# Kernel optimization log

Hardware: AMD Instinct MI355X
Metric: run time of the kernel (lower is better)

Reference implementation:

```python
import jax, jax.numpy as jnp
import numpy as np

B, C_IN, C_OUT, K, IN_SIZE = 16, 32, 32, 16, 8192
OUT_SIZE = IN_SIZE - K  # 8176


def setup_inputs() -> dict:
    key = jax.random.key(0)
    kx, kw, kb = jax.random.split(key, 3)
    x = jax.random.normal(kx, (B, C_IN, IN_SIZE), dtype=jnp.float32)
    # locally-connected (non-weight-shared) conv weights generated by cppn at init
    w = jax.random.normal(kw, (C_OUT, C_IN, OUT_SIZE, K), dtype=jnp.float32)
    b = jax.random.normal(kb, (C_OUT,), dtype=jnp.float32)
    return {"x": x, "w": w, "b": b}


def reference(x, w, b):
    # sliding-window gather: idxs[o, t] = o + t, shape (O, K)
    idxs = jnp.arange(OUT_SIZE)[:, None] + jnp.arange(K)[None, :]
    windows = x[:, :, idxs]  # (B, C_in, O, K)
    # per-output-position weights: contract over C_in and K only
    out = jnp.einsum("bcok,dcok->bdo", windows, w)  # (B, C_out, O)
    return jax.nn.relu(out + b[None, :, None])
```

## Files before the change

### kernel.cpp

```cpp
#include <hip/hip_runtime.h>
#include <cstddef>

constexpr int Bn  = 16;
constexpr int CIc = 32;
constexpr int COc = 32;
constexpr int Kc  = 16;
constexpr int IN  = 8192;
constexpr int OUTL = 8176;

constexpr int O_B  = 16;
constexpr int CCH  = 8;
constexpr int NPOS = O_B + Kc - 1;
constexpr int BST  = 20;

__global__ __launch_bounds__(256, 2)
void conv1d_cppn_kernel(const float* __restrict__ x, const float* __restrict__ w,
                        const float* __restrict__ bias, float* __restrict__ out) {
    __shared__ float xs[CCH][NPOS][BST];

    const int tid = threadIdx.x;
    const int og = tid & 15;
    const int dg = tid >> 4;
    const int o0 = blockIdx.x * O_B;
    const int o  = o0 + og;
    const int dbase = dg * 2;

    float acc[2][16];
#pragma unroll
    for (int i = 0; i < 2; ++i)
#pragma unroll
        for (int j = 0; j < 16; ++j) acc[i][j] = 0.f;

    for (int chunk = 0; chunk < CIc / CCH; ++chunk) {
        const int c0 = chunk * CCH;
        __syncthreads();
        for (int idx = tid; idx < CCH * Bn * NPOS; idx += 256) {
            const int p  = idx % NPOS;
            const int t  = idx / NPOS;
            const int b  = t & 15;
            const int cc = t >> 4;
            xs[cc][p][b] = x[((size_t)b * CIc + (c0 + cc)) * IN + o0 + p];
        }
        __syncthreads();

#pragma unroll 2
        for (int cc = 0; cc < CCH; ++cc) {
            const int c = c0 + cc;
            float wreg[2][16];
#pragma unroll
            for (int jd = 0; jd < 2; ++jd) {
                const float4* wp = reinterpret_cast<const float4*>(
                    w + (((size_t)(dbase + jd) * CIc + c) * OUTL + o) * Kc);
#pragma unroll
                for (int q = 0; q < 4; ++q) {
                    const float4 v = wp[q];
                    wreg[jd][q * 4 + 0] = v.x;
                    wreg[jd][q * 4 + 1] = v.y;
                    wreg[jd][q * 4 + 2] = v.z;
                    wreg[jd][q * 4 + 3] = v.w;
                }
            }
#pragma unroll
            for (int k = 0; k < Kc; ++k) {
                float xv[16];
                *reinterpret_cast<float4*>(&xv[0])  = *reinterpret_cast<const float4*>(&xs[cc][og + k][0]);
                *reinterpret_cast<float4*>(&xv[4])  = *reinterpret_cast<const float4*>(&xs[cc][og + k][4]);
                *reinterpret_cast<float4*>(&xv[8])  = *reinterpret_cast<const float4*>(&xs[cc][og + k][8]);
                *reinterpret_cast<float4*>(&xv[12]) = *reinterpret_cast<const float4*>(&xs[cc][og + k][12]);
#pragma unroll
                for (int jd = 0; jd < 2; ++jd) {
                    const float wk = wreg[jd][k];
#pragma unroll
                    for (int jb = 0; jb < 16; ++jb) {
                        acc[jd][jb] += wk * xv[jb];
                    }
                }
            }
        }
    }

#pragma unroll
    for (int jd = 0; jd < 2; ++jd) {
        const float bv = bias[dbase + jd];
#pragma unroll
        for (int jb = 0; jb < 16; ++jb) {
            float v = acc[jd][jb] + bv;
            out[((size_t)jb * COc + (dbase + jd)) * OUTL + o] = v > 0.f ? v : 0.f;
        }
    }
}

extern "C" void kernel_launch(void* const* d_in, const int* in_sizes, int n_in,
                              void* d_out, int out_size, void* d_ws, size_t ws_size,
                              hipStream_t stream) {
    const float* x    = (const float*)d_in[0];
    const float* w    = (const float*)d_in[1];
    const float* bias = (const float*)d_in[2];
    float* out        = (float*)d_out;

    dim3 grid(OUTL / O_B);
    dim3 block(256);
    hipLaunchKernelGGL(conv1d_cppn_kernel, grid, block, 0, stream, x, w, bias, out);
}
```

Baseline: 121.9 us.

## Split input channels across two thread halves with 4 outputs per thread

```diff
diff --git a/kernel.cpp b/kernel.cpp
--- a/kernel.cpp
+++ b/kernel.cpp
@@ -10,45 +10,48 @@
 
 constexpr int O_B  = 16;
 constexpr int CCH  = 8;
-constexpr int NPOS = O_B + Kc - 1;
+constexpr int NPOS = 32;
 constexpr int BST  = 20;
+
+constexpr int SMEM_FLOATS = 10240;
 
 __global__ __launch_bounds__(256, 2)
 void conv1d_cppn_kernel(const float* __restrict__ x, const float* __restrict__ w,
                         const float* __restrict__ bias, float* __restrict__ out) {
-    __shared__ float xs[CCH][NPOS][BST];
+    __shared__ float smem[SMEM_FLOATS];
+    float (*xs)[CCH][NPOS][BST] = reinterpret_cast<float (*)[CCH][NPOS][BST]>(smem);
+    float (*red)[4][O_B][BST]   = reinterpret_cast<float (*)[4][O_B][BST]>(smem);
 
     const int tid = threadIdx.x;
     const int og = tid & 15;
-    const int dg = tid >> 4;
+    const int dg = (tid >> 4) & 7;
+    const int cg = tid >> 7;
     const int o0 = blockIdx.x * O_B;
     const int o  = o0 + og;
-    const int dbase = dg * 2;
+    const int dbase = dg * 4;
 
-    float acc[2][16];
+    float acc[4][16];
 #pragma unroll
-    for (int i = 0; i < 2; ++i)
+    for (int i = 0; i < 4; ++i)
 #pragma unroll
         for (int j = 0; j < 16; ++j) acc[i][j] = 0.f;
 
-    for (int chunk = 0; chunk < CIc / CCH; ++chunk) {
-        const int c0 = chunk * CCH;
+    for (int it = 0; it < 2; ++it) {
         __syncthreads();
-        for (int idx = tid; idx < CCH * Bn * NPOS; idx += 256) {
-            const int p  = idx % NPOS;
-            const int t  = idx / NPOS;
+        for (int idx = tid; idx < 16 * Bn * NPOS; idx += 256) {
+            const int p  = idx & 31;
+            const int t  = idx >> 5;
             const int b  = t & 15;
-            const int cc = t >> 4;
-            xs[cc][p][b] = x[((size_t)b * CIc + (c0 + cc)) * IN + o0 + p];
+            const int cl = t >> 4;
+            xs[cl >> 3][cl & 7][p][b] = x[((size_t)b * CIc + (it * 16 + cl)) * IN + o0 + p];
         }
         __syncthreads();
 
-#pragma unroll 2
         for (int cc = 0; cc < CCH; ++cc) {
-            const int c = c0 + cc;
-            float wreg[2][16];
+            const int c = it * 16 + cg * 8 + cc;
+            float wreg[4][16];
 #pragma unroll
-            for (int jd = 0; jd < 2; ++jd) {
+            for (int jd = 0; jd < 4; ++jd) {
                 const float4* wp = reinterpret_cast<const float4*>(
                     w + (((size_t)(dbase + jd) * CIc + c) * OUTL + o) * Kc);
 #pragma unroll
@@ -62,13 +65,14 @@
             }
 #pragma unroll
             for (int k = 0; k < Kc; ++k) {
+                const float* xrow = &xs[cg][cc][og + k][0];
                 float xv[16];
-                *reinterpret_cast<float4*>(&xv[0])  = *reinterpret_cast<const float4*>(&xs[cc][og + k][0]);
-                *reinterpret_cast<float4*>(&xv[4])  = *reinterpret_cast<const float4*>(&xs[cc][og + k][4]);
-                *reinterpret_cast<float4*>(&xv[8])  = *reinterpret_cast<const float4*>(&xs[cc][og + k][8]);
-                *reinterpret_cast<float4*>(&xv[12]) = *reinterpret_cast<const float4*>(&xs[cc][og + k][12]);
+                *reinterpret_cast<float4*>(&xv[0])  = *reinterpret_cast<const float4*>(xrow);
+                *reinterpret_cast<float4*>(&xv[4])  = *reinterpret_cast<const float4*>(xrow + 4);
+                *reinterpret_cast<float4*>(&xv[8])  = *reinterpret_cast<const float4*>(xrow + 8);
+                *reinterpret_cast<float4*>(&xv[12]) = *reinterpret_cast<const float4*>(xrow + 12);
 #pragma unroll
-                for (int jd = 0; jd < 2; ++jd) {
+                for (int jd = 0; jd < 4; ++jd) {
                     const float wk = wreg[jd][k];
 #pragma unroll
                     for (int jb = 0; jb < 16; ++jb) {
@@ -79,13 +83,30 @@
         }
     }
 
+    __syncthreads();
+    if (cg == 1) {
 #pragma unroll
-    for (int jd = 0; jd < 2; ++jd) {
-        const float bv = bias[dbase + jd];
+        for (int jd = 0; jd < 4; ++jd) {
+            float* row = &red[dg][jd][og][0];
 #pragma unroll
-        for (int jb = 0; jb < 16; ++jb) {
-            float v = acc[jd][jb] + bv;
-            out[((size_t)jb * COc + (dbase + jd)) * OUTL + o] = v > 0.f ? v : 0.f;
+            for (int q = 0; q < 4; ++q) {
+                *reinterpret_cast<float4*>(row + q * 4) =
+                    make_float4(acc[jd][q * 4 + 0], acc[jd][q * 4 + 1],
+                                acc[jd][q * 4 + 2], acc[jd][q * 4 + 3]);
+            }
+        }
+    }
+    __syncthreads();
+    if (cg == 0) {
+#pragma unroll
+        for (int jd = 0; jd < 4; ++jd) {
+            const float bv = bias[dbase + jd];
+            const float* row = &red[dg][jd][og][0];
+#pragma unroll
+            for (int jb = 0; jb < 16; ++jb) {
+                float v = acc[jd][jb] + row[jb] + bv;
+                out[((size_t)jb * COc + (dbase + jd)) * OUTL + o] = v > 0.f ? v : 0.f;
+            }
         }
     }
 }
```

Measured after the change: 237.4 us. 1.95x slower.

## Double-buffer x tile in LDS with vectorized prefetch into registers

Applied to the files above, without the earlier changes.

```diff
diff --git a/kernel.cpp b/kernel.cpp
--- a/kernel.cpp
+++ b/kernel.cpp
@@ -10,13 +10,14 @@
 
 constexpr int O_B  = 16;
 constexpr int CCH  = 8;
-constexpr int NPOS = O_B + Kc - 1;
+constexpr int NPOS = 32;
 constexpr int BST  = 20;
+constexpr int NCHUNK = CIc / CCH;
 
-__global__ __launch_bounds__(256, 2)
+__global__ __launch_bounds__(256, 3)
 void conv1d_cppn_kernel(const float* __restrict__ x, const float* __restrict__ w,
                         const float* __restrict__ bias, float* __restrict__ out) {
-    __shared__ float xs[CCH][NPOS][BST];
+    __shared__ float xs[2][CCH][NPOS][BST];
 
     const int tid = threadIdx.x;
     const int og = tid & 15;
@@ -25,24 +26,39 @@
     const int o  = o0 + og;
     const int dbase = dg * 2;
 
+    const int sp4 = tid & 7;
+    const int sb  = (tid >> 3) & 15;
+    const int cl0 = tid >> 7;
+
     float acc[2][16];
 #pragma unroll
     for (int i = 0; i < 2; ++i)
 #pragma unroll
         for (int j = 0; j < 16; ++j) acc[i][j] = 0.f;
 
-    for (int chunk = 0; chunk < CIc / CCH; ++chunk) {
+#pragma unroll
+    for (int q = 0; q < 4; ++q) {
+        const int cl = cl0 + 2 * q;
+        const float4 v = *reinterpret_cast<const float4*>(
+            &x[((size_t)sb * CIc + cl) * IN + o0 + sp4 * 4]);
+        float (*prow)[BST] = &xs[0][cl][sp4 * 4];
+        prow[0][sb] = v.x; prow[1][sb] = v.y; prow[2][sb] = v.z; prow[3][sb] = v.w;
+    }
+    __syncthreads();
+
+    int buf = 0;
+    for (int chunk = 0; chunk < NCHUNK; ++chunk) {
+        float4 xr[4];
+        if (chunk + 1 < NCHUNK) {
+            const int c0n = (chunk + 1) * CCH;
+#pragma unroll
+            for (int q = 0; q < 4; ++q) {
+                xr[q] = *reinterpret_cast<const float4*>(
+                    &x[((size_t)sb * CIc + c0n + cl0 + 2 * q) * IN + o0 + sp4 * 4]);
+            }
+        }
+
         const int c0 = chunk * CCH;
-        __syncthreads();
-        for (int idx = tid; idx < CCH * Bn * NPOS; idx += 256) {
-            const int p  = idx % NPOS;
-            const int t  = idx / NPOS;
-            const int b  = t & 15;
-            const int cc = t >> 4;
-            xs[cc][p][b] = x[((size_t)b * CIc + (c0 + cc)) * IN + o0 + p];
-        }
-        __syncthreads();
-
 #pragma unroll 2
         for (int cc = 0; cc < CCH; ++cc) {
             const int c = c0 + cc;
@@ -62,11 +78,12 @@
             }
 #pragma unroll
             for (int k = 0; k < Kc; ++k) {
+                const float* xrow = &xs[buf][cc][og + k][0];
                 float xv[16];
-                *reinterpret_cast<float4*>(&xv[0])  = *reinterpret_cast<const float4*>(&xs[cc][og + k][0]);
-                *reinterpret_cast<float4*>(&xv[4])  = *reinterpret_cast<const float4*>(&xs[cc][og + k][4]);
-                *reinterpret_cast<float4*>(&xv[8])  = *reinterpret_cast<const float4*>(&xs[cc][og + k][8]);
-                *reinterpret_cast<float4*>(&xv[12]) = *reinterpret_cast<const float4*>(&xs[cc][og + k][12]);
+                *reinterpret_cast<float4*>(&xv[0])  = *reinterpret_cast<const float4*>(xrow);
+                *reinterpret_cast<float4*>(&xv[4])  = *reinterpret_cast<const float4*>(xrow + 4);
+                *reinterpret_cast<float4*>(&xv[8])  = *reinterpret_cast<const float4*>(xrow + 8);
+                *reinterpret_cast<float4*>(&xv[12]) = *reinterpret_cast<const float4*>(xrow + 12);
 #pragma unroll
                 for (int jd = 0; jd < 2; ++jd) {
                     const float wk = wreg[jd][k];
@@ -77,6 +94,18 @@
                 }
             }
         }
+
+        if (chunk + 1 < NCHUNK) {
+#pragma unroll
+            for (int q = 0; q < 4; ++q) {
+                const int cl = cl0 + 2 * q;
+                float (*prow)[BST] = &xs[buf ^ 1][cl][sp4 * 4];
+                prow[0][sb] = xr[q].x; prow[1][sb] = xr[q].y;
+                prow[2][sb] = xr[q].z; prow[3][sb] = xr[q].w;
+            }
+            __syncthreads();
+        }
+        buf ^= 1;
     }
 
 #pragma unroll
```

New measurement: 135.7 us. +11.3%, slower.

## Retile threads to 2 outputs x 8 batches with sliding-window x reuse and vectorized staging

Applied to the files above, without the earlier changes.

```diff
diff --git a/kernel.cpp b/kernel.cpp
--- a/kernel.cpp
+++ b/kernel.cpp
@@ -10,8 +10,9 @@
 
 constexpr int O_B  = 16;
 constexpr int CCH  = 8;
-constexpr int NPOS = O_B + Kc - 1;
-constexpr int BST  = 20;
+constexpr int NPOS = 32;
+constexpr int BST  = 18;
+constexpr int NCHUNK = CIc / CCH;
 
 __global__ __launch_bounds__(256, 2)
 void conv1d_cppn_kernel(const float* __restrict__ x, const float* __restrict__ w,
@@ -19,60 +20,85 @@
     __shared__ float xs[CCH][NPOS][BST];
 
     const int tid = threadIdx.x;
-    const int og = tid & 15;
-    const int dg = tid >> 4;
+    const int bg  = tid & 1;
+    const int ogp = (tid >> 1) & 7;
+    const int dg  = tid >> 4;
     const int o0 = blockIdx.x * O_B;
-    const int o  = o0 + og;
+    const int ob = ogp * 2;
+    const int o  = o0 + ob;
     const int dbase = dg * 2;
+    const int bb = bg * 8;
 
-    float acc[2][16];
+    const int sp4 = tid & 7;
+    const int sb  = (tid >> 3) & 15;
+    const int cl0 = tid >> 7;
+
+    float acc[2][2][8];
 #pragma unroll
     for (int i = 0; i < 2; ++i)
 #pragma unroll
-        for (int j = 0; j < 16; ++j) acc[i][j] = 0.f;
+        for (int j = 0; j < 2; ++j)
+#pragma unroll
+            for (int q = 0; q < 8; ++q) acc[i][j][q] = 0.f;
 
-    for (int chunk = 0; chunk < CIc / CCH; ++chunk) {
+    for (int chunk = 0; chunk < NCHUNK; ++chunk) {
         const int c0 = chunk * CCH;
         __syncthreads();
-        for (int idx = tid; idx < CCH * Bn * NPOS; idx += 256) {
-            const int p  = idx % NPOS;
-            const int t  = idx / NPOS;
-            const int b  = t & 15;
-            const int cc = t >> 4;
-            xs[cc][p][b] = x[((size_t)b * CIc + (c0 + cc)) * IN + o0 + p];
+#pragma unroll
+        for (int q = 0; q < 4; ++q) {
+            const int cl = cl0 + 2 * q;
+            const float4 v = *reinterpret_cast<const float4*>(
+                &x[((size_t)sb * CIc + (c0 + cl)) * IN + o0 + sp4 * 4]);
+            float (*prow)[BST] = &xs[cl][sp4 * 4];
+            prow[0][sb] = v.x; prow[1][sb] = v.y; prow[2][sb] = v.z; prow[3][sb] = v.w;
         }
         __syncthreads();
 
 #pragma unroll 2
         for (int cc = 0; cc < CCH; ++cc) {
             const int c = c0 + cc;
-            float wreg[2][16];
+            float xwA[8], xwB[8];
+            *reinterpret_cast<float4*>(&xwA[0]) = *reinterpret_cast<const float4*>(&xs[cc][ob][bb]);
+            *reinterpret_cast<float4*>(&xwA[4]) = *reinterpret_cast<const float4*>(&xs[cc][ob][bb + 4]);
+            *reinterpret_cast<float4*>(&xwB[0]) = *reinterpret_cast<const float4*>(&xs[cc][ob + 1][bb]);
+            *reinterpret_cast<float4*>(&xwB[4]) = *reinterpret_cast<const float4*>(&xs[cc][ob + 1][bb + 4]);
+
 #pragma unroll
-            for (int jd = 0; jd < 2; ++jd) {
-                const float4* wp = reinterpret_cast<const float4*>(
-                    w + (((size_t)(dbase + jd) * CIc + c) * OUTL + o) * Kc);
+            for (int half = 0; half < 2; ++half) {
+                float wv[2][2][8];
 #pragma unroll
-                for (int q = 0; q < 4; ++q) {
-                    const float4 v = wp[q];
-                    wreg[jd][q * 4 + 0] = v.x;
-                    wreg[jd][q * 4 + 1] = v.y;
-                    wreg[jd][q * 4 + 2] = v.z;
-                    wreg[jd][q * 4 + 3] = v.w;
-                }
-            }
+                for (int jd = 0; jd < 2; ++jd)
 #pragma unroll
-            for (int k = 0; k < Kc; ++k) {
-                float xv[16];
-                *reinterpret_cast<float4*>(&xv[0])  = *reinterpret_cast<const float4*>(&xs[cc][og + k][0]);
-                *reinterpret_cast<float4*>(&xv[4])  = *reinterpret_cast<const float4*>(&xs[cc][og + k][4]);
-                *reinterpret_cast<float4*>(&xv[8])  = *reinterpret_cast<const float4*>(&xs[cc][og + k][8]);
-                *reinterpret_cast<float4*>(&xv[12]) = *reinterpret_cast<const float4*>(&xs[cc][og + k][12]);
+                    for (int oo = 0; oo < 2; ++oo) {
+                        const float4* wp = reinterpret_cast<const float4*>(
+                            w + (((size_t)(dbase + jd) * CIc + c) * OUTL + (o + oo)) * Kc
+                              + half * 8);
+                        const float4 a  = wp[0];
+                        const float4 b4 = wp[1];
+                        wv[jd][oo][0] = a.x;  wv[jd][oo][1] = a.y;
+                        wv[jd][oo][2] = a.z;  wv[jd][oo][3] = a.w;
+                        wv[jd][oo][4] = b4.x; wv[jd][oo][5] = b4.y;
+                        wv[jd][oo][6] = b4.z; wv[jd][oo][7] = b4.w;
+                    }
 #pragma unroll
-                for (int jd = 0; jd < 2; ++jd) {
-                    const float wk = wreg[jd][k];
+                for (int kk = 0; kk < 8; ++kk) {
+                    const int k = half * 8 + kk;
 #pragma unroll
-                    for (int jb = 0; jb < 16; ++jb) {
-                        acc[jd][jb] += wk * xv[jb];
+                    for (int jd = 0; jd < 2; ++jd) {
+                        const float wk0 = wv[jd][0][kk];
+                        const float wk1 = wv[jd][1][kk];
+#pragma unroll
+                        for (int j = 0; j < 8; ++j) {
+                            acc[jd][0][j] += wk0 * xwA[j];
+                            acc[jd][1][j] += wk1 * xwB[j];
+                        }
+                    }
+                    if (k < 15) {
+#pragma unroll
+                        for (int j = 0; j < 8; ++j) xwA[j] = xwB[j];
+                        const int r = ob + k + 2;
+                        *reinterpret_cast<float4*>(&xwB[0]) = *reinterpret_cast<const float4*>(&xs[cc][r][bb]);
+                        *reinterpret_cast<float4*>(&xwB[4]) = *reinterpret_cast<const float4*>(&xs[cc][r][bb + 4]);
                     }
                 }
             }
@@ -83,9 +109,12 @@
     for (int jd = 0; jd < 2; ++jd) {
         const float bv = bias[dbase + jd];
 #pragma unroll
-        for (int jb = 0; jb < 16; ++jb) {
-            float v = acc[jd][jb] + bv;
-            out[((size_t)jb * COc + (dbase + jd)) * OUTL + o] = v > 0.f ? v : 0.f;
+        for (int j = 0; j < 8; ++j) {
+            float v0 = acc[jd][0][j] + bv;
+            float v1 = acc[jd][1][j] + bv;
+            float2 st = make_float2(v0 > 0.f ? v0 : 0.f, v1 > 0.f ? v1 : 0.f);
+            *reinterpret_cast<float2*>(
+                &out[((size_t)(bb + j) * COc + (dbase + jd)) * OUTL + o]) = st;
         }
     }
 }
```

Measured after the change: 151.5 us. 1.24x slower.
